# Kernel tuning notes

Measured on AMD Instinct MI355X. Metric: run time of the kernel, lower is better.

The kernel has to match this reference:

```python
import jax, jax.numpy as jnp
import numpy as np

D_MODEL = 768
DT_RANK = D_MODEL // 16  # 48
D_CONV = 4
D_INNER = 2 * D_MODEL    # 1536
D_STATE = 16
BATCH, SEQ_LEN = 1, 4096


def setup_inputs() -> dict:
    key = jax.random.key(0)
    ks = jax.random.split(key, 11)
    def n(k, shape, scale=0.02):
        return jax.random.normal(k, shape, dtype=jnp.float32) * scale
    return {
        "u": jax.random.normal(ks[0], (BATCH, SEQ_LEN, D_MODEL), dtype=jnp.float32),
        "in_proj_w": n(ks[1], (2 * D_INNER, D_MODEL)),
        "conv_w": n(ks[2], (D_INNER, 1, D_CONV)),
        "conv_b": n(ks[3], (D_INNER,)),
        "x_dt_w": n(ks[4], (DT_RANK, D_INNER)),
        "x_b_w": n(ks[5], (D_STATE, D_INNER)),
        "x_c_w": n(ks[6], (D_STATE, D_INNER)),
        "dt_w": n(ks[7], (D_INNER, DT_RANK)),
        "dt_b": n(ks[8], (D_INNER,)),
        # HF Mamba-style S4D-real init: A_log = log(1..N) per channel
        "A_log": jnp.log(jnp.tile(jnp.arange(1, D_STATE + 1, dtype=jnp.float32), (D_INNER, 1))),
        "D_param": jnp.ones((D_INNER,), dtype=jnp.float32),
        "out_proj_w": n(ks[9], (D_MODEL, D_INNER)),
    }


def _silu(x):
    return x * jax.nn.sigmoid(x)


def reference(u, in_proj_w, conv_w, conv_b, x_dt_w, x_b_w, x_c_w,
              dt_w, dt_b, A_log, D_param, out_proj_w):
    batch = u.shape[0]
    # input projection -> x, z  [B, L, D_INNER] each
    xz = u @ in_proj_w.T
    x, z = jnp.split(xz, 2, axis=-1)
    # causal depthwise conv1d over time
    x_ncl = jnp.transpose(x, (0, 2, 1))  # [B, D_INNER, L]
    x_conv = jax.lax.conv_general_dilated(
        x_ncl, conv_w, window_strides=(1,), padding=[(D_CONV - 1, 0)],
        dimension_numbers=("NCH", "OIH", "NCH"), feature_group_count=D_INNER)
    x_conv = x_conv + conv_b[None, :, None]
    x_conv = _silu(jnp.transpose(x_conv, (0, 2, 1)))  # [B, L, D_INNER]
    # data-dependent SSM parameters
    dt_rank = x_conv @ x_dt_w.T                      # [B, L, DT_RANK]
    Bm = x_conv @ x_b_w.T                            # [B, L, D_STATE]
    Cm = x_conv @ x_c_w.T                            # [B, L, D_STATE]
    dt = jax.nn.softplus(dt_rank @ dt_w.T + dt_b)    # [B, L, D_INNER]
    A = -jnp.exp(A_log)                              # [D_INNER, D_STATE]
    dA = jnp.exp(dt[..., None] * A)                  # [B, L, D_INNER, D_STATE]
    dB = dt[..., None] * Bm[:, :, None, :]           # [B, L, D_INNER, D_STATE]

    def step(h, inp):
        dA_t, dB_t, x_t, C_t = inp
        h = h * dA_t + x_t[..., None] * dB_t                 # [B, D_INNER, D_STATE]
        y_t = jnp.sum(h * C_t[:, None, :], axis=-1) + D_param * x_t
        return h, y_t

    h0 = jnp.zeros((batch, D_INNER, D_STATE), dtype=u.dtype)
    scan_inputs = (jnp.moveaxis(dA, 1, 0), jnp.moveaxis(dB, 1, 0),
                   jnp.moveaxis(x_conv, 1, 0), jnp.moveaxis(Cm, 1, 0))
    _, y_ssm = jax.lax.scan(step, h0, scan_inputs)   # [L, B, D_INNER]
    y = jnp.moveaxis(y_ssm, 0, 1) * _silu(z)         # [B, L, D_INNER]
    return y @ out_proj_w.T                          # [B, L, D_MODEL]
```

## Files before the change

kernel.cpp:

```cpp
#include <hip/hip_runtime.h>
#include <math.h>

#define L      4096
#define DM     768
#define DI     1536
#define DS     16
#define DR     48
#define NCOMB  80
#define CH     32
#define NC     128
#define G2_S   16
#define G2_KC  96
#define XZROW  6144

typedef unsigned short u16;
typedef unsigned int   u32;
typedef __attribute__((ext_vector_type(8))) short bf16x8;
typedef __attribute__((ext_vector_type(4))) float f32x4;

__device__ __forceinline__ float silu_f(float v) { return v / (1.f + __expf(-v)); }

__device__ __forceinline__ u16 f2bf(float f) {
    u32 u = __float_as_uint(f);
    return (u16)((u + 0x7fffu + ((u >> 16) & 1u)) >> 16);
}
__device__ __forceinline__ float bf2f(u16 h) {
    return __uint_as_float(((u32)h) << 16);
}

__device__ __forceinline__ float softplus_f(float s) {
    return (s > 20.f) ? s : log1pf(expf(s));
}

__device__ __forceinline__ void gl_lds16(const u16* g, u16* l) {
    __builtin_amdgcn_global_load_lds(
        (const __attribute__((address_space(1))) void*)g,
        (__attribute__((address_space(3))) void*)l, 16, 0, 0);
}

__global__ __launch_bounds__(256)
void gemm_bf16_bt(const u16* __restrict__ A, const u16* __restrict__ W,
                  float* __restrict__ C, int M, int N, int K)
{
    __shared__ u16 As[2][128 * 32];
    __shared__ u16 Bs[2][128 * 32];

    const int tid  = threadIdx.x;
    const int lane = tid & 63;
    const int wave = tid >> 6;
    const int wr   = (wave >> 1) * 64;
    const int wc   = (wave & 1) * 64;
    const int m0   = blockIdx.y * 128;
    const int n0   = blockIdx.x * 128;

    const int r0 = tid >> 2;
    const int k0 = (tid & 3) * 8;

    const int frow = lane & 15;
    const int fk   = (lane >> 4) * 8;

    f32x4 acc[4][4];
    #pragma unroll
    for (int i = 0; i < 4; ++i)
        #pragma unroll
        for (int j = 0; j < 4; ++j)
            acc[i][j] = (f32x4){0.f, 0.f, 0.f, 0.f};

    const int NT = K >> 5;

#define STAGE(buf, kk) {                                                       \
        const u16* ga = A + (size_t)(m0 + r0) * K + (kk) + k0;                 \
        const u16* gw = W + (size_t)(n0 + r0) * K + (kk) + k0;                 \
        gl_lds16(ga,                   &As[buf][tid * 8]);                     \
        gl_lds16(ga + (size_t)64 * K,  &As[buf][2048 + tid * 8]);              \
        gl_lds16(gw,                   &Bs[buf][tid * 8]);                     \
        gl_lds16(gw + (size_t)64 * K,  &Bs[buf][2048 + tid * 8]); }

    STAGE(0, 0);
    __syncthreads();

    for (int t = 0; t < NT; ++t) {
        const int b = t & 1;
        if (t + 1 < NT) STAGE(b ^ 1, (t + 1) << 5);

        bf16x8 af[4], bw[4];
        #pragma unroll
        for (int m = 0; m < 4; ++m)
            af[m] = *(const bf16x8*)&As[b][(wr + m * 16 + frow) * 32 + fk];
        #pragma unroll
        for (int n = 0; n < 4; ++n)
            bw[n] = *(const bf16x8*)&Bs[b][(wc + n * 16 + frow) * 32 + fk];

        #pragma unroll
        for (int m = 0; m < 4; ++m)
            #pragma unroll
            for (int n = 0; n < 4; ++n)
                acc[m][n] = __builtin_amdgcn_mfma_f32_16x16x32_bf16(
                    af[m], bw[n], acc[m][n], 0, 0, 0);

        __syncthreads();
    }
#undef STAGE

    const int crow = (lane >> 4) * 4;
    const int ccol = lane & 15;
    #pragma unroll
    for (int m = 0; m < 4; ++m)
        #pragma unroll
        for (int n = 0; n < 4; ++n)
            #pragma unroll
            for (int r = 0; r < 4; ++r)
                C[(size_t)(m0 + wr + m * 16 + crow + r) * N
                  + n0 + wc + n * 16 + ccol] = acc[m][n][r];
}

__global__ __launch_bounds__(256)
void gemm_bf16_bt_n64(const u16* __restrict__ A, int lda,
                      const u16* __restrict__ W, int ldw,
                      float* __restrict__ C, int M, int N, int K)
{
    __shared__ u16 As[2][128 * 32];
    __shared__ u16 Bs[2][64 * 32];

    const int tid  = threadIdx.x;
    const int lane = tid & 63;
    const int wave = tid >> 6;
    const int wr   = (wave >> 1) * 64;
    const int wc   = (wave & 1) * 32;
    const int m0   = blockIdx.y * 128;
    const int n0   = blockIdx.x * 64;

    const int r0 = tid >> 2;
    const int k0 = (tid & 3) * 8;

    const int frow = lane & 15;
    const int fk   = (lane >> 4) * 8;

    f32x4 acc[4][2];
    #pragma unroll
    for (int i = 0; i < 4; ++i)
        #pragma unroll
        for (int j = 0; j < 2; ++j)
            acc[i][j] = (f32x4){0.f, 0.f, 0.f, 0.f};

    const int NT = K >> 5;

#define STG(buf, kk) {                                                         \
        const u16* ga = A + (size_t)(m0 + r0) * lda + (kk) + k0;               \
        gl_lds16(ga,                     &As[buf][tid * 8]);                   \
        gl_lds16(ga + (size_t)64 * lda,  &As[buf][2048 + tid * 8]);            \
        gl_lds16(W + (size_t)(n0 + r0) * ldw + (kk) + k0, &Bs[buf][tid * 8]); }

    STG(0, 0);
    __syncthreads();

    for (int t = 0; t < NT; ++t) {
        const int b = t & 1;
        if (t + 1 < NT) STG(b ^ 1, (t + 1) << 5);

        bf16x8 af[4], bw[2];
        #pragma unroll
        for (int m = 0; m < 4; ++m)
            af[m] = *(const bf16x8*)&As[b][(wr + m * 16 + frow) * 32 + fk];
        #pragma unroll
        for (int n = 0; n < 2; ++n)
            bw[n] = *(const bf16x8*)&Bs[b][(wc + n * 16 + frow) * 32 + fk];

        #pragma unroll
        for (int m = 0; m < 4; ++m)
            #pragma unroll
            for (int n = 0; n < 2; ++n)
                acc[m][n] = __builtin_amdgcn_mfma_f32_16x16x32_bf16(
                    af[m], bw[n], acc[m][n], 0, 0, 0);

        __syncthreads();
    }
#undef STG

    const int crow = (lane >> 4) * 4;
    const int ccol = lane & 15;
    #pragma unroll
    for (int m = 0; m < 4; ++m)
        #pragma unroll
        for (int n = 0; n < 2; ++n)
            #pragma unroll
            for (int r = 0; r < 4; ++r)
                C[(size_t)(m0 + wr + m * 16 + crow + r) * N
                  + n0 + wc + n * 16 + ccol] = acc[m][n][r];
}

#define NU4  (L * DM / 4)
#define NW4  (2 * DI * DM / 4)
#define NWT  (DI * NCOMB)
#define NA   (DI * DS)
__global__ __launch_bounds__(256)
void pack_early_k(const float* __restrict__ u, const float* __restrict__ Wip,
                  const float* __restrict__ xdt, const float* __restrict__ xb,
                  const float* __restrict__ xc, const float* __restrict__ alog,
                  u16* __restrict__ ubf, u16* __restrict__ Wipb,
                  float* __restrict__ Wt, float* __restrict__ Aneg)
{
    int i = blockIdx.x * 256 + threadIdx.x;
    if (i < NU4) {
        const float4 v = ((const float4*)u)[i];
        ushort4 o; o.x = f2bf(v.x); o.y = f2bf(v.y); o.z = f2bf(v.z); o.w = f2bf(v.w);
        ((ushort4*)ubf)[i] = o;
        return;
    }
    i -= NU4;
    if (i < NW4) {
        const float4 v = ((const float4*)Wip)[i];
        ushort4 o; o.x = f2bf(v.x); o.y = f2bf(v.y); o.z = f2bf(v.z); o.w = f2bf(v.w);
        ((ushort4*)Wipb)[i] = o;
        return;
    }
    i -= NW4;
    if (i < NWT) {
        const int k = i / NCOMB, n = i - k * NCOMB;
        float v;
        if (n < 48)      v = xdt[n * DI + k];
        else if (n < 64) v = xb[(n - 48) * DI + k];
        else             v = xc[(n - 64) * DI + k];
        Wt[i] = v;
        return;
    }
    i -= NWT;
    if (i < NA)
        Aneg[i] = -expf(alog[i]);
}

#define NO4  (DM * DI / 4)
__global__ __launch_bounds__(256)
void pack_wop_k(const float* __restrict__ Wop, u16* __restrict__ xzu)
{
    int i = blockIdx.x * 256 + threadIdx.x;
    if (i >= NO4) return;
    const float4 v = ((const float4*)Wop)[i];
    ushort4 o; o.x = f2bf(v.x); o.y = f2bf(v.y); o.z = f2bf(v.z); o.w = f2bf(v.w);
    const int e = i * 4;
    const int r = e / DI, c = e - r * DI;
    *(ushort4*)(xzu + (size_t)r * XZROW + 1536 + c) = o;
}

__global__ __launch_bounds__(256)
void conv_silu_v4(const float* __restrict__ xz, const float* __restrict__ cw,
                  const float* __restrict__ cb, float* __restrict__ xcv)
{
    int idx = blockIdx.x * 256 + threadIdx.x;
    if (idx >= L * (DI / 4)) return;
    const int t = idx / (DI / 4);
    const int q = idx - t * (DI / 4);
    const int d = q * 4;

    const float4 w0 = ((const float4*)cw)[d + 0];
    const float4 w1 = ((const float4*)cw)[d + 1];
    const float4 w2 = ((const float4*)cw)[d + 2];
    const float4 w3 = ((const float4*)cw)[d + 3];
    float4 acc = ((const float4*)cb)[q];

    const float* base = xz + d;
    #pragma unroll
    for (int j = 0; j < 4; ++j) {
        const int tt = t - 3 + j;
        if (tt >= 0) {
            const float4 x = *(const float4*)(base + (size_t)tt * (2 * DI));
            acc.x = fmaf(((const float*)&w0)[j], x.x, acc.x);
            acc.y = fmaf(((const float*)&w1)[j], x.y, acc.y);
            acc.z = fmaf(((const float*)&w2)[j], x.z, acc.z);
            acc.w = fmaf(((const float*)&w3)[j], x.w, acc.w);
        }
    }
    float4 o;
    o.x = silu_f(acc.x); o.y = silu_f(acc.y);
    o.z = silu_f(acc.z); o.w = silu_f(acc.w);
    ((float4*)xcv)[idx] = o;
}

__global__ __launch_bounds__(256)
void gemm2_splitk(const float* __restrict__ A, const float* __restrict__ Wt,
                  float* __restrict__ part)
{
    __shared__ float As[G2_KC][65];
    __shared__ float Ws[G2_KC][80];

    const int tid  = threadIdx.x;
    const int m0   = blockIdx.x * 64;
    const int koff = blockIdx.y * G2_KC;

    {
        const int r = tid >> 2, cg = tid & 3;
        #pragma unroll
        for (int j = 0; j < 6; ++j) {
            const int kk = (j * 4 + cg) * 4;
            const float4 v = *(const float4*)(A + (size_t)(m0 + r) * DI + koff + kk);
            As[kk + 0][r] = v.x; As[kk + 1][r] = v.y;
            As[kk + 2][r] = v.z; As[kk + 3][r] = v.w;
        }
    }
    for (int i = tid; i < G2_KC * 80; i += 256)
        (&Ws[0][0])[i] = Wt[(size_t)koff * 80 + i];
    __syncthreads();

    const int g  = tid >> 6;
    const int r  = tid & 63;
    const int c0 = g * 20;

    float acc[20];
    #pragma unroll
    for (int j = 0; j < 20; ++j) acc[j] = 0.f;

    #pragma unroll 2
    for (int k = 0; k < G2_KC; ++k) {
        const float a = As[k][r];
        #pragma unroll
        for (int q = 0; q < 5; ++q) {
            const float4 w = *(const float4*)&Ws[k][c0 + q * 4];
            acc[q * 4 + 0] = fmaf(a, w.x, acc[q * 4 + 0]);
            acc[q * 4 + 1] = fmaf(a, w.y, acc[q * 4 + 1]);
            acc[q * 4 + 2] = fmaf(a, w.z, acc[q * 4 + 2]);
            acc[q * 4 + 3] = fmaf(a, w.w, acc[q * 4 + 3]);
        }
    }

    float* p = part + (size_t)blockIdx.y * (L * NCOMB)
                    + (size_t)(m0 + r) * NCOMB + c0;
    #pragma unroll
    for (int q = 0; q < 5; ++q)
        ((float4*)p)[q] = make_float4(acc[q * 4], acc[q * 4 + 1],
                                      acc[q * 4 + 2], acc[q * 4 + 3]);
}

__global__ __launch_bounds__(256)
void gemm2_reduce(const float* __restrict__ part, float* __restrict__ dtbc)
{
    int i = blockIdx.x * 256 + threadIdx.x;
    if (i >= L * NCOMB) return;
    float s = 0.f;
    #pragma unroll
    for (int j = 0; j < G2_S; ++j)
        s += part[(size_t)j * L * NCOMB + i];
    dtbc[i] = s;
}

__global__ __launch_bounds__(256)
void dt_k(const float* __restrict__ dtbc, const float* __restrict__ dtw,
          const float* __restrict__ dtb, u16* __restrict__ dt)
{
    __shared__ float dtr_s[32][48];
    const int tid = threadIdx.x;
    const int d   = blockIdx.x * 256 + tid;
    const int t0  = blockIdx.y * 32;

    for (int i = tid; i < 384; i += 256) {
        const int r = i / 12, c = (i - r * 12) * 4;
        const float4 v = *(const float4*)(dtbc + (size_t)(t0 + r) * NCOMB + c);
        *(float4*)&dtr_s[r][c] = v;
    }
    __syncthreads();

    float w[48];
    #pragma unroll
    for (int j = 0; j < 12; ++j) {
        const float4 v = *(const float4*)(dtw + (size_t)d * DR + j * 4);
        w[j * 4 + 0] = v.x; w[j * 4 + 1] = v.y;
        w[j * 4 + 2] = v.z; w[j * 4 + 3] = v.w;
    }
    const float b = dtb[d];

    for (int t = 0; t < 32; ++t) {
        float s = b;
        #pragma unroll
        for (int j = 0; j < 12; ++j) {
            const float4 v = *(const float4*)&dtr_s[t][j * 4];
            s = fmaf(v.x, w[j * 4 + 0], s);
            s = fmaf(v.y, w[j * 4 + 1], s);
            s = fmaf(v.z, w[j * 4 + 2], s);
            s = fmaf(v.w, w[j * 4 + 3], s);
        }
        dt[(size_t)(t0 + t) * DI + d] = f2bf(softplus_f(s));
    }
}

__global__ __launch_bounds__(256)
void scan1_k(const u16* __restrict__ dt, const float* __restrict__ xcv,
             const float* __restrict__ dtbc, const float* __restrict__ Aneg,
             u16* __restrict__ hloc, float* __restrict__ Ssum)
{
    __shared__ float Bs[CH][DS];
    const int c = blockIdx.y;
    const int d = blockIdx.x * 256 + threadIdx.x;

    for (int i = threadIdx.x; i < CH * DS; i += 256) {
        int tt = i >> 4, n = i & 15;
        Bs[tt][n] = dtbc[(size_t)(c * CH + tt) * NCOMB + 48 + n];
    }
    __syncthreads();

    float Ad[DS], h[DS];
    #pragma unroll
    for (int q = 0; q < 4; ++q)
        *(float4*)&Ad[q * 4] = *(const float4*)(Aneg + (size_t)d * DS + q * 4);
    #pragma unroll
    for (int n = 0; n < DS; ++n) h[n] = 0.f;

    size_t base = (size_t)(c * CH) * DI + d;
    float S = 0.f;
    for (int tt = 0; tt < CH; ++tt, base += DI) {
        const float dtv = bf2f(dt[base]);
        const float xv  = xcv[base];
        S += dtv;
        const float xdt = xv * dtv;
        #pragma unroll
        for (int n = 0; n < DS; ++n)
            h[n] = fmaf(h[n], __expf(Ad[n] * dtv), xdt * Bs[tt][n]);
    }

    u16* o = hloc + ((size_t)c * DI + d) * DS;
    #pragma unroll
    for (int q = 0; q < 4; ++q) {
        ushort4 pk;
        pk.x = f2bf(h[q * 4 + 0]); pk.y = f2bf(h[q * 4 + 1]);
        pk.z = f2bf(h[q * 4 + 2]); pk.w = f2bf(h[q * 4 + 3]);
        *(ushort4*)(o + q * 4) = pk;
    }
    Ssum[c * DI + d] = S;
}

__global__ __launch_bounds__(256)
void scan2_k(u16* hc, const float* __restrict__ Ssum,
             const float* __restrict__ Aneg)
{
    const int p = blockIdx.x * 256 + threadIdx.x;
    if (p >= DI * DS) return;
    const int d = p >> 4;
    const float Ad = Aneg[p];
    float h = 0.f;
    for (int c = 0; c < NC; ++c) {
        const size_t o = (size_t)c * DI * DS + p;
        const float hl = bf2f(hc[o]);
        hc[o] = f2bf(h);
        h = fmaf(h, __expf(Ad * Ssum[c * DI + d]), hl);
    }
}

__global__ __launch_bounds__(256)
void scan3_k(const u16* __restrict__ dt, const float* __restrict__ xcv,
             const float* __restrict__ dtbc, const float* __restrict__ Aneg,
             const u16* __restrict__ carry, const float* __restrict__ Dp,
             const float* __restrict__ xz, u16* __restrict__ ybf)
{
    __shared__ float Bs[CH][DS];
    __shared__ float Cs[CH][DS];
    const int c = blockIdx.y;
    const int d = blockIdx.x * 256 + threadIdx.x;

    for (int i = threadIdx.x; i < CH * DS; i += 256) {
        int tt = i >> 4, n = i & 15;
        Bs[tt][n] = dtbc[(size_t)(c * CH + tt) * NCOMB + 48 + n];
        Cs[tt][n] = dtbc[(size_t)(c * CH + tt) * NCOMB + 64 + n];
    }
    __syncthreads();

    float Ad[DS], h[DS];
    const u16* co = carry + ((size_t)c * DI + d) * DS;
    #pragma unroll
    for (int q = 0; q < 4; ++q) {
        const ushort4 cv = *(const ushort4*)(co + q * 4);
        h[q * 4 + 0] = bf2f(cv.x); h[q * 4 + 1] = bf2f(cv.y);
        h[q * 4 + 2] = bf2f(cv.z); h[q * 4 + 3] = bf2f(cv.w);
    }
    #pragma unroll
    for (int q = 0; q < 4; ++q)
        *(float4*)&Ad[q * 4] = *(const float4*)(Aneg + (size_t)d * DS + q * 4);
    const float Dv = Dp[d];

    int t = c * CH;
    for (int tt = 0; tt < CH; ++tt, ++t) {
        const size_t o = (size_t)t * DI + d;
        const float dtv = bf2f(dt[o]);
        const float xv  = xcv[o];
        const float xdt = xv * dtv;
        float y = Dv * xv;
        #pragma unroll
        for (int n = 0; n < DS; ++n) {
            h[n] = fmaf(h[n], __expf(Ad[n] * dtv), xdt * Bs[tt][n]);
            y = fmaf(h[n], Cs[tt][n], y);
        }
        const float z = xz[(size_t)t * (2 * DI) + DI + d];
        ybf[(size_t)t * XZROW + d] = f2bf(y * silu_f(z));
    }
}

extern "C" void kernel_launch(void* const* d_in, const int* in_sizes, int n_in,
                              void* d_out, int out_size, void* d_ws, size_t ws_size,
                              hipStream_t stream)
{
    const float* u    = (const float*)d_in[0];
    const float* Wip  = (const float*)d_in[1];
    const float* cw   = (const float*)d_in[2];
    const float* cb   = (const float*)d_in[3];
    const float* xdt  = (const float*)d_in[4];
    const float* xbw  = (const float*)d_in[5];
    const float* xcw  = (const float*)d_in[6];
    const float* dtw  = (const float*)d_in[7];
    const float* dtb  = (const float*)d_in[8];
    const float* alog = (const float*)d_in[9];
    const float* Dp   = (const float*)d_in[10];
    const float* Wop  = (const float*)d_in[11];
    float* out = (float*)d_out;

    float* ws   = (float*)d_ws;
    float* xz   = ws;
    float* xcv  = xz   + (size_t)L * 2 * DI;
    float* dtbc = xcv  + (size_t)L * DI;
    float* dty  = dtbc + (size_t)L * NCOMB;
    float* Wt   = dty  + (size_t)L * DI;
    u16*   hc   = (u16*)(Wt + (size_t)DI * NCOMB);
    float* Ssum = Wt + (size_t)DI * NCOMB
                     + (size_t)NC * DI * DS / 2;
    float* Aneg = Ssum + (size_t)NC * DI;

    u16*   ubf  = (u16*)xcv;
    u16*   Wipb = (u16*)xcv + (size_t)L * DM;
    float* g2p  = dty;
    u16*   dtbf = (u16*)dty;
    u16*   xzu  = (u16*)xz;

    const dim3 blk(256);

    pack_early_k<<<(NU4 + NW4 + NWT + NA + 255) / 256, blk, 0, stream>>>(
        u, Wip, xdt, xbw, xcw, alog, ubf, Wipb, Wt, Aneg);

    gemm_bf16_bt<<<dim3((2 * DI) / 128, L / 128), blk, 0, stream>>>(
        ubf, Wipb, xz, L, 2 * DI, DM);

    conv_silu_v4<<<(L * (DI / 4) + 255) / 256, blk, 0, stream>>>(xz, cw, cb, xcv);

    pack_wop_k<<<(NO4 + 255) / 256, blk, 0, stream>>>(Wop, xzu);

    gemm2_splitk<<<dim3(L / 64, G2_S), blk, 0, stream>>>(xcv, Wt, g2p);
    gemm2_reduce<<<(L * NCOMB + 255) / 256, blk, 0, stream>>>(g2p, dtbc);

    dt_k<<<dim3(DI / 256, L / 32), blk, 0, stream>>>(dtbc, dtw, dtb, dtbf);

    scan1_k<<<dim3(DI / 256, NC), blk, 0, stream>>>(
        dtbf, xcv, dtbc, Aneg, hc, Ssum);
    scan2_k<<<(DI * DS) / 256, blk, 0, stream>>>(hc, Ssum, Aneg);
    scan3_k<<<dim3(DI / 256, NC), blk, 0, stream>>>(
        dtbf, xcv, dtbc, Aneg, hc, Dp, xz, xzu);

    gemm_bf16_bt_n64<<<dim3(DM / 64, L / 128), blk, 0, stream>>>(
        xzu, XZROW, xzu + 1536, XZROW, out, L, DM, DI);
}
```

Measured before the change: 237.3 us.

## Store xz and conv output in bf16, fold Wop packing into early pack

The in_proj GEMM now writes bf16 instead of fp32. The conv/SiLU output is stored as bf16 too, and conv, the split-K GEMM, scan1 and scan3 read these halved buffers. The out_proj weight packing moves into the early pack kernel with its own buffer, which removes one launch, and the workspace layout changes to fit. The aim is to cut memory traffic across the memory-bound elementwise and scan kernels, at the cost of lower precision on the intermediates. The y output overwrites the x half of the xz buffer in place while z is still read from the same rows.

Result: faster. 230.9 us (-2.7%).

```diff
diff --git a/kernel.cpp b/kernel.cpp
--- a/kernel.cpp
+++ b/kernel.cpp
@@ -11,7 +11,7 @@
 #define NC     128
 #define G2_S   16
 #define G2_KC  96
-#define XZROW  6144
+#define XZROW  3072
 
 typedef unsigned short u16;
 typedef unsigned int   u32;
@@ -39,8 +39,8 @@
 }
 
 __global__ __launch_bounds__(256)
-void gemm_bf16_bt(const u16* __restrict__ A, const u16* __restrict__ W,
-                  float* __restrict__ C, int M, int N, int K)
+void gemm_bf16_bt_o16(const u16* __restrict__ A, const u16* __restrict__ W,
+                      u16* __restrict__ Cb, int M, int N, int K)
 {
     __shared__ u16 As[2][128 * 32];
     __shared__ u16 Bs[2][128 * 32];
@@ -110,8 +110,8 @@
         for (int n = 0; n < 4; ++n)
             #pragma unroll
             for (int r = 0; r < 4; ++r)
-                C[(size_t)(m0 + wr + m * 16 + crow + r) * N
-                  + n0 + wc + n * 16 + ccol] = acc[m][n][r];
+                Cb[(size_t)(m0 + wr + m * 16 + crow + r) * N
+                   + n0 + wc + n * 16 + ccol] = f2bf(acc[m][n][r]);
 }
 
 __global__ __launch_bounds__(256)
@@ -191,13 +191,16 @@
 
 #define NU4  (L * DM / 4)
 #define NW4  (2 * DI * DM / 4)
+#define NO4  (DM * DI / 4)
 #define NWT  (DI * NCOMB)
 #define NA   (DI * DS)
 __global__ __launch_bounds__(256)
 void pack_early_k(const float* __restrict__ u, const float* __restrict__ Wip,
+                  const float* __restrict__ Wop,
                   const float* __restrict__ xdt, const float* __restrict__ xb,
                   const float* __restrict__ xc, const float* __restrict__ alog,
                   u16* __restrict__ ubf, u16* __restrict__ Wipb,
+                  u16* __restrict__ wopb,
                   float* __restrict__ Wt, float* __restrict__ Aneg)
 {
     int i = blockIdx.x * 256 + threadIdx.x;
@@ -215,6 +218,13 @@
         return;
     }
     i -= NW4;
+    if (i < NO4) {
+        const float4 v = ((const float4*)Wop)[i];
+        ushort4 o; o.x = f2bf(v.x); o.y = f2bf(v.y); o.z = f2bf(v.z); o.w = f2bf(v.w);
+        ((ushort4*)wopb)[i] = o;
+        return;
+    }
+    i -= NO4;
     if (i < NWT) {
         const int k = i / NCOMB, n = i - k * NCOMB;
         float v;
@@ -229,22 +239,9 @@
         Aneg[i] = -expf(alog[i]);
 }
 
-#define NO4  (DM * DI / 4)
-__global__ __launch_bounds__(256)
-void pack_wop_k(const float* __restrict__ Wop, u16* __restrict__ xzu)
-{
-    int i = blockIdx.x * 256 + threadIdx.x;
-    if (i >= NO4) return;
-    const float4 v = ((const float4*)Wop)[i];
-    ushort4 o; o.x = f2bf(v.x); o.y = f2bf(v.y); o.z = f2bf(v.z); o.w = f2bf(v.w);
-    const int e = i * 4;
-    const int r = e / DI, c = e - r * DI;
-    *(ushort4*)(xzu + (size_t)r * XZROW + 1536 + c) = o;
-}
-
-__global__ __launch_bounds__(256)
-void conv_silu_v4(const float* __restrict__ xz, const float* __restrict__ cw,
-                  const float* __restrict__ cb, float* __restrict__ xcv)
+__global__ __launch_bounds__(256)
+void conv_silu_v4(const u16* __restrict__ xzb, const float* __restrict__ cw,
+                  const float* __restrict__ cb, u16* __restrict__ xcvb)
 {
     int idx = blockIdx.x * 256 + threadIdx.x;
     if (idx >= L * (DI / 4)) return;
@@ -258,26 +255,26 @@
     const float4 w3 = ((const float4*)cw)[d + 3];
     float4 acc = ((const float4*)cb)[q];
 
-    const float* base = xz + d;
+    const u16* base = xzb + d;
     #pragma unroll
     for (int j = 0; j < 4; ++j) {
         const int tt = t - 3 + j;
         if (tt >= 0) {
-            const float4 x = *(const float4*)(base + (size_t)tt * (2 * DI));
-            acc.x = fmaf(((const float*)&w0)[j], x.x, acc.x);
-            acc.y = fmaf(((const float*)&w1)[j], x.y, acc.y);
-            acc.z = fmaf(((const float*)&w2)[j], x.z, acc.z);
-            acc.w = fmaf(((const float*)&w3)[j], x.w, acc.w);
+            const ushort4 xb4 = *(const ushort4*)(base + (size_t)tt * XZROW);
+            acc.x = fmaf(((const float*)&w0)[j], bf2f(xb4.x), acc.x);
+            acc.y = fmaf(((const float*)&w1)[j], bf2f(xb4.y), acc.y);
+            acc.z = fmaf(((const float*)&w2)[j], bf2f(xb4.z), acc.z);
+            acc.w = fmaf(((const float*)&w3)[j], bf2f(xb4.w), acc.w);
         }
     }
-    float4 o;
-    o.x = silu_f(acc.x); o.y = silu_f(acc.y);
-    o.z = silu_f(acc.z); o.w = silu_f(acc.w);
-    ((float4*)xcv)[idx] = o;
-}
-
-__global__ __launch_bounds__(256)
-void gemm2_splitk(const float* __restrict__ A, const float* __restrict__ Wt,
+    ushort4 o;
+    o.x = f2bf(silu_f(acc.x)); o.y = f2bf(silu_f(acc.y));
+    o.z = f2bf(silu_f(acc.z)); o.w = f2bf(silu_f(acc.w));
+    ((ushort4*)xcvb)[idx] = o;
+}
+
+__global__ __launch_bounds__(256)
+void gemm2_splitk(const u16* __restrict__ A, const float* __restrict__ Wt,
                   float* __restrict__ part)
 {
     __shared__ float As[G2_KC][65];
@@ -292,9 +289,9 @@
         #pragma unroll
         for (int j = 0; j < 6; ++j) {
             const int kk = (j * 4 + cg) * 4;
-            const float4 v = *(const float4*)(A + (size_t)(m0 + r) * DI + koff + kk);
-            As[kk + 0][r] = v.x; As[kk + 1][r] = v.y;
-            As[kk + 2][r] = v.z; As[kk + 3][r] = v.w;
+            const ushort4 v = *(const ushort4*)(A + (size_t)(m0 + r) * DI + koff + kk);
+            As[kk + 0][r] = bf2f(v.x); As[kk + 1][r] = bf2f(v.y);
+            As[kk + 2][r] = bf2f(v.z); As[kk + 3][r] = bf2f(v.w);
         }
     }
     for (int i = tid; i < G2_KC * 80; i += 256)
@@ -382,7 +379,7 @@
 }
 
 __global__ __launch_bounds__(256)
-void scan1_k(const u16* __restrict__ dt, const float* __restrict__ xcv,
+void scan1_k(const u16* __restrict__ dt, const u16* __restrict__ xcv,
              const float* __restrict__ dtbc, const float* __restrict__ Aneg,
              u16* __restrict__ hloc, float* __restrict__ Ssum)
 {
@@ -407,7 +404,7 @@
     float S = 0.f;
     for (int tt = 0; tt < CH; ++tt, base += DI) {
         const float dtv = bf2f(dt[base]);
-        const float xv  = xcv[base];
+        const float xv  = bf2f(xcv[base]);
         S += dtv;
         const float xdt = xv * dtv;
         #pragma unroll
@@ -444,10 +441,10 @@
 }
 
 __global__ __launch_bounds__(256)
-void scan3_k(const u16* __restrict__ dt, const float* __restrict__ xcv,
+void scan3_k(const u16* __restrict__ dt, const u16* __restrict__ xcv,
              const float* __restrict__ dtbc, const float* __restrict__ Aneg,
              const u16* __restrict__ carry, const float* __restrict__ Dp,
-             const float* __restrict__ xz, u16* __restrict__ ybf)
+             const u16* __restrict__ xzb, u16* __restrict__ ybf)
 {
     __shared__ float Bs[CH][DS];
     __shared__ float Cs[CH][DS];
@@ -478,7 +475,7 @@
     for (int tt = 0; tt < CH; ++tt, ++t) {
         const size_t o = (size_t)t * DI + d;
         const float dtv = bf2f(dt[o]);
-        const float xv  = xcv[o];
+        const float xv  = bf2f(xcv[o]);
         const float xdt = xv * dtv;
         float y = Dv * xv;
         #pragma unroll
@@ -486,7 +483,7 @@
             h[n] = fmaf(h[n], __expf(Ad[n] * dtv), xdt * Bs[tt][n]);
             y = fmaf(h[n], Cs[tt][n], y);
         }
-        const float z = xz[(size_t)t * (2 * DI) + DI + d];
+        const float z = bf2f(xzb[(size_t)t * XZROW + DI + d]);
         ybf[(size_t)t * XZROW + d] = f2bf(y * silu_f(z));
     }
 }
@@ -510,45 +507,45 @@
     float* out = (float*)d_out;
 
     float* ws   = (float*)d_ws;
-    float* xz   = ws;
-    float* xcv  = xz   + (size_t)L * 2 * DI;
-    float* dtbc = xcv  + (size_t)L * DI;
+    u16*   xzb  = (u16*)ws;
+    u16*   xcvb = (u16*)(ws + (size_t)L * XZROW / 2);
+    float* dtbc = ws + (size_t)L * XZROW / 2
+                     + (size_t)L * DI / 2;
     float* dty  = dtbc + (size_t)L * NCOMB;
     float* Wt   = dty  + (size_t)L * DI;
     u16*   hc   = (u16*)(Wt + (size_t)DI * NCOMB);
     float* Ssum = Wt + (size_t)DI * NCOMB
                      + (size_t)NC * DI * DS / 2;
     float* Aneg = Ssum + (size_t)NC * DI;
-
-    u16*   ubf  = (u16*)xcv;
-    u16*   Wipb = (u16*)xcv + (size_t)L * DM;
+    u16*   wopb = (u16*)(Aneg + NA);
+
+    u16*   ubf  = xcvb;
+    u16*   Wipb = xcvb + (size_t)L * DM;
     float* g2p  = dty;
     u16*   dtbf = (u16*)dty;
-    u16*   xzu  = (u16*)xz;
+    u16*   ybf  = xzb;
 
     const dim3 blk(256);
 
-    pack_early_k<<<(NU4 + NW4 + NWT + NA + 255) / 256, blk, 0, stream>>>(
-        u, Wip, xdt, xbw, xcw, alog, ubf, Wipb, Wt, Aneg);
-
-    gemm_bf16_bt<<<dim3((2 * DI) / 128, L / 128), blk, 0, stream>>>(
-        ubf, Wipb, xz, L, 2 * DI, DM);
-
-    conv_silu_v4<<<(L * (DI / 4) + 255) / 256, blk, 0, stream>>>(xz, cw, cb, xcv);
-
-    pack_wop_k<<<(NO4 + 255) / 256, blk, 0, stream>>>(Wop, xzu);
-
-    gemm2_splitk<<<dim3(L / 64, G2_S), blk, 0, stream>>>(xcv, Wt, g2p);
+    pack_early_k<<<(NU4 + NW4 + NO4 + NWT + NA + 255) / 256, blk, 0, stream>>>(
+        u, Wip, Wop, xdt, xbw, xcw, alog, ubf, Wipb, wopb, Wt, Aneg);
+
+    gemm_bf16_bt_o16<<<dim3((2 * DI) / 128, L / 128), blk, 0, stream>>>(
+        ubf, Wipb, xzb, L, 2 * DI, DM);
+
+    conv_silu_v4<<<(L * (DI / 4) + 255) / 256, blk, 0, stream>>>(xzb, cw, cb, xcvb);
+
+    gemm2_splitk<<<dim3(L / 64, G2_S), blk, 0, stream>>>(xcvb, Wt, g2p);
     gemm2_reduce<<<(L * NCOMB + 255) / 256, blk, 0, stream>>>(g2p, dtbc);
 
     dt_k<<<dim3(DI / 256, L / 32), blk, 0, stream>>>(dtbc, dtw, dtb, dtbf);
 
     scan1_k<<<dim3(DI / 256, NC), blk, 0, stream>>>(
-        dtbf, xcv, dtbc, Aneg, hc, Ssum);
+        dtbf, xcvb, dtbc, Aneg, hc, Ssum);
     scan2_k<<<(DI * DS) / 256, blk, 0, stream>>>(hc, Ssum, Aneg);
     scan3_k<<<dim3(DI / 256, NC), blk, 0, stream>>>(
-        dtbf, xcv, dtbc, Aneg, hc, Dp, xz, xzu);
+        dtbf, xcvb, dtbc, Aneg, hc, Dp, xzb, ybf);
 
     gemm_bf16_bt_n64<<<dim3(DM / 64, L / 128), blk, 0, stream>>>(
-        xzu, XZROW, xzu + 1536, XZROW, out, L, DM, DI);
-}
+        ybf, XZROW, wopb, DI, out, L, DM, DI);
+}
```
